# Performance work log

Measured on AMD Instinct MI355X. Metric: run time of the kernel, lower is better.

## Reference

```python
import jax, jax.numpy as jnp
import numpy as np

B, HH, WW, E = 8, 64, 64, 384
NH, EXP = 6, 2
D1 = (EXP * E) // NH * NH      # 768
HD = D1 // NH                  # 128
RPE = 512
LAYERS = 3
EPS = 1e-6


def srms(x):
    # SimpleRMSNorm: no learnable weight
    return x * jax.lax.rsqrt(jnp.mean(x * x, axis=-1, keepdims=True) + EPS)


def rpe_forward(pos, pw, pb, lw, lb, ow, ob):
    # pos: (n, 1) -> (n, NH*HD). Rpe MLP: act(pos_proj) -> layers x [norm,act,linear] -> out
    x = jax.nn.relu(pos @ pw + pb)
    for i in range(lw.shape[0]):  # fixed small layer count
        x = jax.nn.relu(srms(x)) @ lw[i] + lb[i]
    return jax.nn.relu(srms(x)) @ ow + ob


def tno_coeffs(n, pw, pb, lw, lb, ow, ob):
    # Toeplitz coeffs t_0..t_{n-1}, t_0(dummy), t_{-(n-1)}..t_{-1} for circular conv of len 2n
    pos = jnp.arange(1, n, dtype=jnp.float32)[:, None]             # (n-1, 1), par_type=1
    neg = -jnp.arange(1, n, dtype=jnp.float32)[::-1][:, None]      # -(n-1)..-1
    zero = jnp.zeros((1, 1), dtype=jnp.float32)
    t_zero = rpe_forward(zero, pw, pb, lw, lb, ow, ob)             # (1, NH*HD)
    t_pos = rpe_forward(pos, pw, pb, lw, lb, ow, ob)               # (n-1, NH*HD)
    t_neg = rpe_forward(neg, pw, pb, lw, lb, ow, ob)
    a = jnp.concatenate([t_zero, t_pos, t_zero, t_neg], axis=0)    # (2n, NH*HD)
    return a.reshape(2 * n, NH, HD).transpose(1, 0, 2)             # (NH, 2n, HD)


def tno_apply(v, a, axis):
    # v: (b, h, H, W, d); FFT-based Toeplitz (circular) mixing along `axis` in {-3, -2}
    n = v.shape[axis]
    a = a[:, :, None, :] if axis == -3 else a[:, None, :, :]
    y = jnp.fft.rfft(v, 2 * n, axis=axis)
    af = jnp.fft.rfft(a, 2 * n, axis=axis)
    out = jnp.fft.irfft(af * y, 2 * n, axis=axis)
    return jax.lax.slice_in_dim(out, 0, n, axis=out.ndim + axis)


def setup_inputs() -> dict:
    key = jax.random.key(0)
    ks = jax.random.split(key, 24)
    s = 0.02
    def rn(k, shape):
        return jax.random.normal(k, shape, dtype=jnp.float32) * s
    inp = {
        "x": jax.random.normal(ks[0], (B, HH, WW, E), dtype=jnp.float32),
        "H": HH, "W": WW,
        "Wu": rn(ks[1], (E, D1)), "bu": jnp.zeros((D1,), jnp.float32),
        "Wv": rn(ks[2], (E, D1)), "bv": jnp.zeros((D1,), jnp.float32),
        "Wo": rn(ks[3], (D1, E)), "bo": jnp.zeros((E,), jnp.float32),
    }
    for t, off in (("r1", 4), ("r2", 10)):
        inp[t + "_pw"] = rn(ks[off], (1, RPE))
        inp[t + "_pb"] = jnp.zeros((RPE,), jnp.float32)
        inp[t + "_lw"] = rn(ks[off + 1], (LAYERS, RPE, RPE))
        inp[t + "_lb"] = jnp.zeros((LAYERS, RPE), jnp.float32)
        inp[t + "_ow"] = rn(ks[off + 2], (RPE, NH * HD))
        inp[t + "_ob"] = jnp.zeros((NH * HD,), jnp.float32)
    return inp


def reference(x, H, W, Wu, bu, Wv, bv, Wo, bo,
              r1_pw, r1_pb, r1_lw, r1_lb, r1_ow, r1_ob,
              r2_pw, r2_pb, r2_lw, r2_lb, r2_ow, r2_ob):
    b = x.shape[0]
    xn = srms(x)                                    # pre_norm (SimpleRMSNorm)
    u = jax.nn.silu(xn @ Wu + bu)                   # gate branch
    v = jax.nn.silu(xn @ Wv + bv)
    v = v.reshape(b, H, W, NH, HD).transpose(0, 3, 1, 2, 4)        # b h H W d
    a_h = tno_coeffs(H, r2_pw, r2_pb, r2_lw, r2_lb, r2_ow, r2_ob)  # toep2, dim=-3
    a_w = tno_coeffs(W, r1_pw, r1_pb, r1_lw, r1_lb, r1_ow, r1_ob)  # toep1, dim=-2
    out = tno_apply(v, a_h, -3) + tno_apply(v, a_w, -2)
    out = out.transpose(0, 2, 3, 1, 4).reshape(b, H, W, NH * HD)   # b H W (h d)
    out = u * out
    return out @ Wo + bo + x
```

## Files before the change

### kernel.cpp

```cpp
#include <hip/hip_runtime.h>
#include <stdint.h>


typedef __attribute__((ext_vector_type(4))) float  f32x4;
typedef __attribute__((ext_vector_type(8))) short  s16x8;
typedef __attribute__((ext_vector_type(8))) unsigned short u16x8;
typedef __attribute__((ext_vector_type(4))) unsigned short u16x4;
typedef unsigned short u16;

#define M_TOT 32768

__device__ __forceinline__ u16 f2bf(float f) {
  union { float f; unsigned int u; } v; v.f = f;
  unsigned int r = (v.u + 0x7FFFu + ((v.u >> 16) & 1u)) >> 16;
  return (u16)r;
}
__device__ __forceinline__ float bf2f(u16 h) {
  union { unsigned int u; float f; } v; v.u = ((unsigned int)h) << 16;
  return v.f;
}
__device__ __forceinline__ float silu_f(float x) {
  return x * __builtin_amdgcn_rcpf(1.f + __expf(-x));
}

__device__ __forceinline__ void gload_lds16(const u16* g, u16* l) {
  __builtin_amdgcn_global_load_lds(
      (const __attribute__((address_space(1))) uint32_t*)g,
      (__attribute__((address_space(3))) uint32_t*)l, 16, 0, 0);
}

__global__ __launch_bounds__(256) void setup_k(
    const float* __restrict__ x, u16* __restrict__ xn,
    const float* __restrict__ Wu, const float* __restrict__ Wv,
    const float* __restrict__ Wo, u16* __restrict__ Wuvt, u16* __restrict__ Wot,
    const float* __restrict__ r1lw, const float* __restrict__ r1ow,
    const float* __restrict__ r2lw, const float* __restrict__ r2ow,
    u16* __restrict__ lwT, u16* __restrict__ owT,
    const float* __restrict__ r1pw, const float* __restrict__ r1pb,
    const float* __restrict__ r2pw, const float* __restrict__ r2pb,
    float* __restrict__ X0) {
  __shared__ float sm[32][33];
  const int bid = blockIdx.x;
  const int tid = threadIdx.x;

  if (bid < 8192) {
    int row  = bid * 4 + (tid >> 6);
    int lane = tid & 63;
    const float* xr = x + (size_t)row * 384 + lane;
    float v[6]; float ss = 0.f;
#pragma unroll
    for (int i = 0; i < 6; i++) { v[i] = xr[i * 64]; ss += v[i] * v[i]; }
#pragma unroll
    for (int off = 32; off > 0; off >>= 1) ss += __shfl_xor(ss, off);
    float sc = rsqrtf(ss * (1.f / 384.f) + 1e-6f);
    u16* o = xn + (size_t)row * 384 + lane;
#pragma unroll
    for (int i = 0; i < 6; i++) o[i * 64] = f2bf(v[i] * sc);
  } else if (bid < 11360) {
    int b = bid - 8192;
    const float* src; u16* dst; int C, DS, R0, C0;
    if (b < 2304) {
      int mlp = b / 1152, r = b % 1152;
      if (r < 768) {
        int L = r / 256, t = r % 256;
        R0 = (t / 16) * 32; C0 = (t % 16) * 32;
        src = (mlp ? r2lw : r1lw) + (size_t)L * 262144;
        dst = lwT + (size_t)(mlp * 3 + L) * 262144;
        C = 512; DS = 512;
      } else {
        int t = r - 768;
        R0 = (t / 24) * 32; C0 = (t % 24) * 32;
        src = mlp ? r2ow : r1ow;
        dst = owT + (size_t)mlp * 393216;
        C = 768; DS = 512;
      }
    } else {
      int t = b - 2304;
      if (t < 288)      { R0 = (t / 24) * 32; C0 = (t % 24) * 32;
                          src = Wu; C = 768; dst = Wuvt;             DS = 384; }
      else if (t < 576) { int t2 = t - 288; R0 = (t2 / 24) * 32; C0 = (t2 % 24) * 32;
                          src = Wv; C = 768; dst = Wuvt + 768 * 384; DS = 384; }
      else              { int t2 = t - 576; R0 = (t2 / 12) * 32; C0 = (t2 % 12) * 32;
                          src = Wo; C = 384; dst = Wot;              DS = 768; }
    }
    int lx = tid % 32, ly = tid / 32;
#pragma unroll
    for (int q = 0; q < 4; q++) {
      int y = q * 8 + ly;
      sm[y][lx] = src[(size_t)(R0 + y) * C + C0 + lx];
    }
    __syncthreads();
#pragma unroll
    for (int q = 0; q < 4; q++) {
      int y = q * 8 + ly;
      dst[(size_t)(C0 + y) * DS + R0 + lx] = f2bf(sm[lx][y]);
    }
  } else {
    int idx = (bid - 11360) * 256 + tid;
    int gid = idx * 4;
    int row = gid >> 9, col = gid & 511;
    int mlp = row >> 7, p = row & 127;
    float pos = (p < 64) ? (float)p : ((p == 64) ? 0.f : (float)(p - 128));
    const float* pw = (mlp ? r2pw : r1pw) + col;
    const float* pb = (mlp ? r2pb : r1pb) + col;
    f32x4 w = *(const f32x4*)pw;
    f32x4 bb = *(const f32x4*)pb;
    f32x4 o;
#pragma unroll
    for (int e = 0; e < 4; e++) o[e] = fmaxf(pos * w[e] + bb[e], 0.f);
    *(f32x4*)(X0 + gid) = o;
  }
}

template <int N, bool TOUT>
__global__ __launch_bounds__(256) void rpe_layer_k(
    const float* __restrict__ X,
    const u16* __restrict__ wtA, const u16* __restrict__ wtB,
    const float* __restrict__ bA, const float* __restrict__ bB,
    float* __restrict__ outA, float* __restrict__ outB) {
  constexpr int NT = N / 128;
  const int mlp = blockIdx.x / NT;
  const int n0  = (blockIdx.x % NT) * 128;
  const u16* WT = mlp ? wtB : wtA;
  const float* bias = mlp ? bB : bA;
  float* out = mlp ? outB : outA;
  const float* Xm = X + (size_t)mlp * 128 * 512;

  __shared__ float scale[128];
  __shared__ __align__(16) u16 As[128 * 64];
  __shared__ __align__(16) u16 Bs[128 * 64];

  const int tid  = threadIdx.x;
  const int lane = tid & 63;
  const int wid  = tid >> 6;
  const int wm   = wid >> 1, wn = wid & 1;
  const int fl   = lane & 15, fh = lane >> 4;

  {
    int row = tid >> 1, half = tid & 1;
    const float* xr = Xm + (size_t)row * 512 + half * 256;
    float ss = 0.f;
#pragma unroll 8
    for (int q = 0; q < 64; q++) {
      f32x4 v = *(const f32x4*)(xr + q * 4);
      ss += v[0] * v[0] + v[1] * v[1] + v[2] * v[2] + v[3] * v[3];
    }
    ss += __shfl_xor(ss, 1);
    if (!half) scale[row] = rsqrtf(ss * (1.f / 512.f) + 1e-6f);
  }
  __syncthreads();

  f32x4 acc[4][4];
  {
    f32x4 z = {0.f, 0.f, 0.f, 0.f};
#pragma unroll
    for (int i = 0; i < 4; i++)
#pragma unroll
      for (int j = 0; j < 4; j++) acc[i][j] = z;
  }

  const int arow = tid >> 1, acb = (tid & 1) * 32;
  const int sr = tid >> 3, sc = (tid & 7) * 8;

  for (int kt = 0; kt < 512; kt += 64) {
    {
      const float* xp = Xm + (size_t)arow * 512 + kt + acb;
      float s_ = scale[arow];
      u16* dst = As + arow * 64 + acb;
#pragma unroll
      for (int q = 0; q < 8; q++) {
        f32x4 v = *(const f32x4*)(xp + q * 4);
        u16x4 pk;
#pragma unroll
        for (int e = 0; e < 4; e++) pk[e] = f2bf(fmaxf(v[e], 0.f) * s_);
        *(u16x4*)(dst + q * 4) = pk;
      }
    }
    {
      const u16* gB = WT + (size_t)(n0 + sr) * 512 + kt + sc;
      u16* lB = Bs + sr * 64 + sc;
#pragma unroll
      for (int i = 0; i < 4; i++)
        gload_lds16(gB + (size_t)(i * 32) * 512, lB + i * 32 * 64);
    }
    __syncthreads();
#pragma unroll
    for (int ks = 0; ks < 2; ks++) {
      s16x8 af[4], bfr[4];
      const u16* ap = As + (wm * 64 + fl) * 64 + ks * 32 + fh * 8;
      const u16* bp = Bs + (wn * 64 + fl) * 64 + ks * 32 + fh * 8;
#pragma unroll
      for (int i = 0; i < 4; i++) af[i] = *(const s16x8*)(ap + i * 16 * 64);
#pragma unroll
      for (int j = 0; j < 4; j++) bfr[j] = *(const s16x8*)(bp + j * 16 * 64);
#pragma unroll
      for (int i = 0; i < 4; i++)
#pragma unroll
        for (int j = 0; j < 4; j++)
          acc[i][j] = __builtin_amdgcn_mfma_f32_16x16x32_bf16(af[i], bfr[j], acc[i][j], 0, 0, 0);
    }
    __syncthreads();
  }

#pragma unroll
  for (int i = 0; i < 4; i++)
#pragma unroll
    for (int j = 0; j < 4; j++) {
      int c = n0 + wn * 64 + j * 16 + fl;
      float bv_ = bias[c];
#pragma unroll
      for (int q = 0; q < 4; q++) {
        int r = wm * 64 + i * 16 + fh * 4 + q;
        if (TOUT) out[(size_t)c * 128 + r] = acc[i][j][q] + bv_;
        else      out[(size_t)r * N + c]   = acc[i][j][q] + bv_;
      }
    }
}

__global__ __launch_bounds__(256) void gemm0_k(
    const u16* __restrict__ A, const u16* __restrict__ Bt,
    u16* __restrict__ u_out, u16* __restrict__ vt_out,
    const float* __restrict__ bu, const float* __restrict__ bv) {
  __shared__ __align__(16) char smem[34816];
  u16*   As  = (u16*)smem;
  u16*   Bs  = As + 128 * 64;
  float* epi = (float*)smem;

  const int tid  = threadIdx.x;
  const int lane = tid & 63;
  const int wid  = tid >> 6;
  const int wm   = wid >> 1, wn = wid & 1;
  const int bm   = blockIdx.x & 255, bn = blockIdx.x >> 8;
  const int m0   = bm * 128, n0 = bn * 128;
  const int fl   = lane & 15, fh = lane >> 4;
  const int K    = 384;

  f32x4 acc[4][4];
  {
    f32x4 z = {0.f, 0.f, 0.f, 0.f};
#pragma unroll
    for (int i = 0; i < 4; i++)
#pragma unroll
      for (int j = 0; j < 4; j++) acc[i][j] = z;
  }

  const int sr  = tid >> 3;
  const int scl = (tid & 7) * 8;
  const int scs = ((tid & 7) ^ (sr & 7)) * 8;

  for (int kt = 0; kt < K; kt += 64) {
    const u16* gA = A  + (size_t)(m0 + sr) * K + kt + scs;
    const u16* gB = Bt + (size_t)(n0 + sr) * K + kt + scs;
    u16* lA = As + sr * 64 + scl;
    u16* lB = Bs + sr * 64 + scl;
#pragma unroll
    for (int i = 0; i < 4; i++) {
      gload_lds16(gA + (size_t)(i * 32) * K, lA + i * 32 * 64);
      gload_lds16(gB + (size_t)(i * 32) * K, lB + i * 32 * 64);
    }
    __syncthreads();
#pragma unroll
    for (int ks = 0; ks < 2; ks++) {
      s16x8 af[4], bfr[4];
      const int xc = ((ks * 4 + fh) ^ (fl & 7)) * 8;
      const u16* ap = As + (wm * 64 + fl) * 64 + xc;
      const u16* bp = Bs + (wn * 64 + fl) * 64 + xc;
#pragma unroll
      for (int i = 0; i < 4; i++) af[i] = *(const s16x8*)(ap + i * 16 * 64);
#pragma unroll
      for (int j = 0; j < 4; j++) bfr[j] = *(const s16x8*)(bp + j * 16 * 64);
#pragma unroll
      for (int i = 0; i < 4; i++)
#pragma unroll
        for (int j = 0; j < 4; j++)
          acc[i][j] = __builtin_amdgcn_mfma_f32_16x16x32_bf16(af[i], bfr[j], acc[i][j], 0, 0, 0);
    }
    __syncthreads();
  }

  for (int half = 0; half < 2; half++) {
    __syncthreads();
    if (wm == half) {
#pragma unroll
      for (int i = 0; i < 4; i++)
#pragma unroll
        for (int j = 0; j < 4; j++) {
          int er = i * 16 + fh * 4;
          int ec = wn * 64 + j * 16 + fl;
#pragma unroll
          for (int q = 0; q < 4; q++) epi[(er + q) * 132 + ec] = acc[i][j][q];
        }
    }
    __syncthreads();
    const bool isU = (n0 < 768);
    u16* baseo = isU ? u_out : vt_out;
    const int cc = tid >> 1;
    const int cg = (isU ? n0 : n0 - 768) + cc;
    const float bias_v = (isU ? bu : bv)[cg];
    u16* dst = baseo + (size_t)cg * M_TOT + m0 + half * 64;
#pragma unroll
    for (int q = 0; q < 4; q++) {
      int mb = (tid & 1) * 8 + q * 16;
      u16x8 pk;
#pragma unroll
      for (int e = 0; e < 8; e++) {
        int mm = mb + e;
        pk[e] = f2bf(silu_f(epi[mm * 132 + cc] + bias_v));
      }
      *(u16x8*)(dst + mb) = pk;
    }
  }
}

__global__ __launch_bounds__(512, 2) void gemm2_k(
    const u16* __restrict__ gT, const u16* __restrict__ Wot,
    float* __restrict__ out, const float* __restrict__ bo,
    const float* __restrict__ xres) {
  __shared__ __align__(16) u16 As[128 * 64];
  __shared__ __align__(16) u16 Bs[384 * 64];

  const int tid  = threadIdx.x;
  const int lane = tid & 63;
  const int wid  = tid >> 6;
  const int wm   = wid >> 2;
  const int wn   = wid & 3;
  const int m0   = blockIdx.x * 128;
  const int fl   = lane & 15, fh = lane >> 4;

  f32x4 acc[4][6];
  {
    f32x4 z = {0.f, 0.f, 0.f, 0.f};
#pragma unroll
    for (int i = 0; i < 4; i++)
#pragma unroll
      for (int j = 0; j < 6; j++) acc[i][j] = z;
  }

  const int sr  = tid >> 3;
  const int scl = (tid & 7) * 8;
  const int scs = ((tid & 7) ^ (sr & 7)) * 8;
  const int cr  = tid & 63;
  const int mw  = (tid >> 6) * 16;
  const int c8  = cr >> 3, of = cr & 7;

  for (int kt = 0; kt < 768; kt += 64) {
#pragma unroll
    for (int i = 0; i < 6; i++)
      gload_lds16(Wot + (size_t)(sr + 64 * i) * 768 + kt + scs,
                  Bs + (sr + 64 * i) * 64 + scl);
    {
      const u16* ga = gT + (size_t)(kt + cr) * M_TOT + m0 + mw;
      u16x8 r0 = *(const u16x8*)ga;
      u16x8 r1 = *(const u16x8*)(ga + 8);
#pragma unroll
      for (int e = 0; e < 8; e++)
        As[(mw + e) * 64 + ((c8 ^ e) << 3) + of] = r0[e];
#pragma unroll
      for (int e = 0; e < 8; e++)
        As[(mw + 8 + e) * 64 + ((c8 ^ e) << 3) + of] = r1[e];
    }
    __syncthreads();
#pragma unroll
    for (int ks = 0; ks < 2; ks++) {
      s16x8 af[4], bfr[6];
      const int xc = ((ks * 4 + fh) ^ (fl & 7)) * 8;
      const u16* ap = As + (wm * 64 + fl) * 64 + xc;
      const u16* bp = Bs + (wn * 96 + fl) * 64 + xc;
#pragma unroll
      for (int i = 0; i < 4; i++) af[i] = *(const s16x8*)(ap + i * 16 * 64);
#pragma unroll
      for (int j = 0; j < 6; j++) bfr[j] = *(const s16x8*)(bp + j * 16 * 64);
#pragma unroll
      for (int i = 0; i < 4; i++)
#pragma unroll
        for (int j = 0; j < 6; j++)
          acc[i][j] = __builtin_amdgcn_mfma_f32_16x16x32_bf16(af[i], bfr[j], acc[i][j], 0, 0, 0);
    }
    __syncthreads();
  }

  float bov[6];
#pragma unroll
  for (int j = 0; j < 6; j++) bov[j] = bo[wn * 96 + j * 16 + fl];
#pragma unroll
  for (int i = 0; i < 4; i++) {
#pragma unroll
    for (int q = 0; q < 4; q++) {
      int m = m0 + wm * 64 + i * 16 + fh * 4 + q;
      const float* xr = xres + (size_t)m * 384;
      float* orow = out + (size_t)m * 384;
#pragma unroll
      for (int j = 0; j < 6; j++) {
        int n = wn * 96 + j * 16 + fl;
        orow[n] = acc[i][j][q] + bov[j] + xr[n];
      }
    }
  }
}

__global__ __launch_bounds__(256) void conv_k(const u16* __restrict__ vt,
                                              const u16* __restrict__ ut,
                                              const float* __restrict__ a_hT,
                                              const float* __restrict__ a_wT,
                                              u16* __restrict__ gT) {
  __shared__ __align__(16) u16 Th[64 * 72];
  __shared__ __align__(16) u16 Tw[64 * 72];
  __shared__ __align__(16) u16 Vs[64 * 72];
  __shared__ __align__(16) u16 VTs[64 * 72];
  __shared__ __align__(16) u16 Us[64 * 72];
  __shared__ float ahr[192];
  __shared__ float awr[192];
  u16* epi = VTs;

  const int tid = threadIdx.x;
  const int c = blockIdx.x;
  const int lane = tid & 63, w = tid >> 6;
  const int fl = lane & 15, fh = lane >> 4;

  if (tid < 192) {
    int idx = (128 - tid) & 127;
    ahr[tid] = a_hT[(size_t)c * 128 + idx];
    awr[tid] = a_wT[(size_t)c * 128 + idx];
  }
  __syncthreads();

  {
    int y = tid & 63, j0 = (tid >> 6) * 16;
    int base = 128 - y + j0;
    u16x8 p0, p1, q0, q1;
#pragma unroll
    for (int e = 0; e < 8; e++) {
      p0[e] = f2bf(ahr[base + e]);
      p1[e] = f2bf(ahr[base + 8 + e]);
      q0[e] = f2bf(awr[base + e]);
      q1[e] = f2bf(awr[base + 8 + e]);
    }
    *(u16x8*)(Th + y * 72 + j0)     = p0;
    *(u16x8*)(Th + y * 72 + j0 + 8) = p1;
    *(u16x8*)(Tw + y * 72 + j0)     = q0;
    *(u16x8*)(Tw + y * 72 + j0 + 8) = q1;
  }

  const int sy = tid >> 2, sx = (tid & 3) * 16;
  const int ty = tid & 63, tj = (tid >> 6) * 16;

  for (int b = 0; b < 8; b++) {
    const u16* srcv = vt + (size_t)c * M_TOT + b * 4096;
    const u16* srcu = ut + (size_t)c * M_TOT + b * 4096;
    *(u16x8*)(Vs + sy * 72 + sx)     = *(const u16x8*)(srcv + sy * 64 + sx);
    *(u16x8*)(Vs + sy * 72 + sx + 8) = *(const u16x8*)(srcv + sy * 64 + sx + 8);
    *(u16x8*)(Us + sy * 72 + sx)     = *(const u16x8*)(srcu + sy * 64 + sx);
    *(u16x8*)(Us + sy * 72 + sx + 8) = *(const u16x8*)(srcu + sy * 64 + sx + 8);
    __syncthreads();

    {
      u16x8 q0 = *(const u16x8*)(Vs + ty * 72 + tj);
      u16x8 q1 = *(const u16x8*)(Vs + ty * 72 + tj + 8);
#pragma unroll
      for (int e = 0; e < 8; e++) VTs[(tj + e) * 72 + ty]     = q0[e];
#pragma unroll
      for (int e = 0; e < 8; e++) VTs[(tj + 8 + e) * 72 + ty] = q1[e];
    }
    __syncthreads();

    f32x4 acc[4];
    {
      f32x4 z = {0.f, 0.f, 0.f, 0.f};
#pragma unroll
      for (int i = 0; i < 4; i++) acc[i] = z;
    }
#pragma unroll
    for (int ks = 0; ks < 2; ks++) {
      s16x8 qh = *(const s16x8*)(Th + (w * 16 + fl) * 72 + ks * 32 + fh * 8);
#pragma unroll
      for (int i = 0; i < 4; i++) {
        s16x8 p = *(const s16x8*)(VTs + (i * 16 + fl) * 72 + ks * 32 + fh * 8);
        acc[i] = __builtin_amdgcn_mfma_f32_16x16x32_bf16(p, qh, acc[i], 0, 0, 0);
      }
      s16x8 qw = *(const s16x8*)(Vs + (w * 16 + fl) * 72 + ks * 32 + fh * 8);
#pragma unroll
      for (int i = 0; i < 4; i++) {
        s16x8 p = *(const s16x8*)(Tw + (i * 16 + fl) * 72 + ks * 32 + fh * 8);
        acc[i] = __builtin_amdgcn_mfma_f32_16x16x32_bf16(p, qw, acc[i], 0, 0, 0);
      }
    }
    __syncthreads();

    {
      int y = w * 16 + fl;
#pragma unroll
      for (int i = 0; i < 4; i++) {
        u16x4 uq = *(const u16x4*)(Us + y * 72 + i * 16 + fh * 4);
        u16x4 pk;
#pragma unroll
        for (int e = 0; e < 4; e++) pk[e] = f2bf(acc[i][e] * bf2f(uq[e]));
        *(u16x4*)(epi + y * 72 + i * 16 + fh * 4) = pk;
      }
    }
    __syncthreads();

    {
      u16x8 a0 = *(const u16x8*)(epi + sy * 72 + sx);
      u16x8 a1 = *(const u16x8*)(epi + sy * 72 + sx + 8);
      u16* dst = gT + (size_t)c * M_TOT + b * 4096 + sy * 64 + sx;
      *(u16x8*)dst = a0;
      *(u16x8*)(dst + 8) = a1;
    }
    __syncthreads();
  }
}

extern "C" void kernel_launch(void* const* d_in, const int* in_sizes, int n_in,
                              void* d_out, int out_size, void* d_ws, size_t ws_size,
                              hipStream_t stream) {
  const float* x    = (const float*)d_in[0];
  const float* Wu   = (const float*)d_in[3];
  const float* bu   = (const float*)d_in[4];
  const float* Wv   = (const float*)d_in[5];
  const float* bv   = (const float*)d_in[6];
  const float* Wo   = (const float*)d_in[7];
  const float* bo   = (const float*)d_in[8];
  const float* r1pw = (const float*)d_in[9];
  const float* r1pb = (const float*)d_in[10];
  const float* r1lw = (const float*)d_in[11];
  const float* r1lb = (const float*)d_in[12];
  const float* r1ow = (const float*)d_in[13];
  const float* r1ob = (const float*)d_in[14];
  const float* r2pw = (const float*)d_in[15];
  const float* r2pb = (const float*)d_in[16];
  const float* r2lw = (const float*)d_in[17];
  const float* r2lb = (const float*)d_in[18];
  const float* r2ow = (const float*)d_in[19];
  const float* r2ob = (const float*)d_in[20];
  float* outp = (float*)d_out;

  char* ws = (char*)d_ws;
  size_t off = 0;
  auto carve = [&](size_t bytes) {
    char* p = ws + off;
    off += (bytes + 255) & ~(size_t)255;
    return p;
  };
  u16*   xn   = (u16*)carve((size_t)M_TOT * 384 * 2);
  u16*   uT   = (u16*)carve((size_t)768 * M_TOT * 2);
  u16*   vT   = (u16*)carve((size_t)768 * M_TOT * 2);
  u16*   gT   = (u16*)carve((size_t)768 * M_TOT * 2);
  u16*   Wuvt = (u16*)carve((size_t)1536 * 384 * 2);
  u16*   Wot  = (u16*)carve((size_t)384 * 768 * 2);
  float* awT  = (float*)carve((size_t)768 * 128 * 4);
  float* ahT  = (float*)carve((size_t)768 * 128 * 4);

  char* rb  = (char*)gT;
  u16*   lwT = (u16*)rb;
  u16*   owT = (u16*)(rb + 3145728);
  float* X0  = (float*)(rb + 3145728 + 1572864);
  float* X1  = X0 + 256 * 512;

  setup_k<<<11488, 256, 0, stream>>>(x, xn, Wu, Wv, Wo, Wuvt, Wot,
                                     r1lw, r1ow, r2lw, r2ow, lwT, owT,
                                     r1pw, r1pb, r2pw, r2pb, X0);

  rpe_layer_k<512, false><<<8, 256, 0, stream>>>(X0, lwT, lwT + 3 * 262144,
                                                 r1lb, r2lb, X1, X1 + 128 * 512);
  rpe_layer_k<512, false><<<8, 256, 0, stream>>>(X1, lwT + 262144, lwT + 4 * 262144,
                                                 r1lb + 512, r2lb + 512, X0, X0 + 128 * 512);
  rpe_layer_k<512, false><<<8, 256, 0, stream>>>(X0, lwT + 2 * 262144, lwT + 5 * 262144,
                                                 r1lb + 1024, r2lb + 1024, X1, X1 + 128 * 512);
  rpe_layer_k<768, true><<<12, 256, 0, stream>>>(X1, owT, owT + 393216,
                                                 r1ob, r2ob, awT, ahT);

  gemm0_k<<<256 * 12, 256, 0, stream>>>(xn, Wuvt, uT, vT, bu, bv);
  conv_k<<<768, 256, 0, stream>>>(vT, uT, ahT, awT, gT);
  gemm2_k<<<256, 512, 0, stream>>>(gT, Wot, outp, bo, x);
}
```

Before: 395.9 us.

## Restructure RPE layer kernel with full weight slice in LDS and double-buffered A

The RPE MLP layer kernel now uses 64-column output slices, which doubles the grid from 8/12 to 16/24 blocks. Each block preloads its whole 64x512 weight slice into LDS with an XOR swizzle, and double-buffers the normalized activation tiles with register prefetch, so only one barrier is needed per k-step. The gemm2 A-tile transpose load is also reworked to issue one 16-byte load per thread per pass, with each lane reading a different M chunk. The aim is better parallelism in tiny, latency-bound kernels and fewer LDS bank conflicts, at the cost of more LDS per block.

```diff
diff --git a/kernel.cpp b/kernel.cpp
--- a/kernel.cpp
+++ b/kernel.cpp
@@ -118,23 +118,30 @@
     const u16* __restrict__ wtA, const u16* __restrict__ wtB,
     const float* __restrict__ bA, const float* __restrict__ bB,
     float* __restrict__ outA, float* __restrict__ outB) {
-  constexpr int NT = N / 128;
-  const int mlp = blockIdx.x / NT;
-  const int n0  = (blockIdx.x % NT) * 128;
+  constexpr int NSL = N / 64;
+  const int mlp = blockIdx.x / NSL;
+  const int n0  = (blockIdx.x % NSL) * 64;
   const u16* WT = mlp ? wtB : wtA;
   const float* bias = mlp ? bB : bA;
   float* out = mlp ? outB : outA;
   const float* Xm = X + (size_t)mlp * 128 * 512;
 
+  __shared__ __align__(16) u16 Bs[64 * 512];
+  __shared__ __align__(16) u16 As[2][128 * 64];
   __shared__ float scale[128];
-  __shared__ __align__(16) u16 As[128 * 64];
-  __shared__ __align__(16) u16 Bs[128 * 64];
 
   const int tid  = threadIdx.x;
   const int lane = tid & 63;
-  const int wid  = tid >> 6;
-  const int wm   = wid >> 1, wn = wid & 1;
+  const int w    = tid >> 6;
   const int fl   = lane & 15, fh = lane >> 4;
+
+#pragma unroll
+  for (int r = 0; r < 16; r++) {
+    int row  = r * 4 + w;
+    int csrc = (lane & ~7) | ((lane & 7) ^ (row & 7));
+    gload_lds16(WT + (size_t)(n0 + row) * 512 + csrc * 8,
+                Bs + row * 512 + lane * 8);
+  }
 
   {
     int row = tid >> 1, half = tid & 1;
@@ -150,67 +157,89 @@
   }
   __syncthreads();
 
-  f32x4 acc[4][4];
+  int arow[4], akc[4];
+  float s_[4];
+#pragma unroll
+  for (int q = 0; q < 4; q++) {
+    int cid = q * 256 + tid;
+    arow[q] = cid >> 3;
+    akc[q]  = cid & 7;
+    s_[q]   = scale[arow[q]];
+  }
+
+#pragma unroll
+  for (int q = 0; q < 4; q++) {
+    const float* xp = Xm + (size_t)arow[q] * 512 + akc[q] * 8;
+    f32x4 v0 = *(const f32x4*)xp;
+    f32x4 v1 = *(const f32x4*)(xp + 4);
+    u16x8 pk;
+#pragma unroll
+    for (int e = 0; e < 4; e++) pk[e]     = f2bf(fmaxf(v0[e], 0.f) * s_[q]);
+#pragma unroll
+    for (int e = 0; e < 4; e++) pk[4 + e] = f2bf(fmaxf(v1[e], 0.f) * s_[q]);
+    *(u16x8*)(&As[0][arow[q] * 64 + ((akc[q] ^ (arow[q] & 7)) * 8)]) = pk;
+  }
+  __syncthreads();
+
+  f32x4 acc[2][4];
   {
     f32x4 z = {0.f, 0.f, 0.f, 0.f};
 #pragma unroll
-    for (int i = 0; i < 4; i++)
+    for (int i = 0; i < 2; i++)
 #pragma unroll
       for (int j = 0; j < 4; j++) acc[i][j] = z;
   }
 
-  const int arow = tid >> 1, acb = (tid & 1) * 32;
-  const int sr = tid >> 3, sc = (tid & 7) * 8;
-
-  for (int kt = 0; kt < 512; kt += 64) {
-    {
-      const float* xp = Xm + (size_t)arow * 512 + kt + acb;
-      float s_ = scale[arow];
-      u16* dst = As + arow * 64 + acb;
-#pragma unroll
-      for (int q = 0; q < 8; q++) {
-        f32x4 v = *(const f32x4*)(xp + q * 4);
-        u16x4 pk;
-#pragma unroll
-        for (int e = 0; e < 4; e++) pk[e] = f2bf(fmaxf(v[e], 0.f) * s_);
-        *(u16x4*)(dst + q * 4) = pk;
-      }
-    }
-    {
-      const u16* gB = WT + (size_t)(n0 + sr) * 512 + kt + sc;
-      u16* lB = Bs + sr * 64 + sc;
-#pragma unroll
-      for (int i = 0; i < 4; i++)
-        gload_lds16(gB + (size_t)(i * 32) * 512, lB + i * 32 * 64);
-    }
-    __syncthreads();
+  for (int kti = 0; kti < 8; kti++) {
+    const int cur = kti & 1;
+    f32x4 pf0[4], pf1[4];
+    if (kti < 7) {
+#pragma unroll
+      for (int q = 0; q < 4; q++) {
+        const float* xp = Xm + (size_t)arow[q] * 512 + (kti + 1) * 64 + akc[q] * 8;
+        pf0[q] = *(const f32x4*)xp;
+        pf1[q] = *(const f32x4*)(xp + 4);
+      }
+    }
 #pragma unroll
     for (int ks = 0; ks < 2; ks++) {
-      s16x8 af[4], bfr[4];
-      const u16* ap = As + (wm * 64 + fl) * 64 + ks * 32 + fh * 8;
-      const u16* bp = Bs + (wn * 64 + fl) * 64 + ks * 32 + fh * 8;
-#pragma unroll
-      for (int i = 0; i < 4; i++) af[i] = *(const s16x8*)(ap + i * 16 * 64);
-#pragma unroll
-      for (int j = 0; j < 4; j++) bfr[j] = *(const s16x8*)(bp + j * 16 * 64);
-#pragma unroll
-      for (int i = 0; i < 4; i++)
+      const int xc = ((ks * 4 + fh) ^ (fl & 7)) * 8;
+      s16x8 af[2], bfr[4];
+#pragma unroll
+      for (int i = 0; i < 2; i++)
+        af[i] = *(const s16x8*)(&As[cur][(w * 32 + i * 16 + fl) * 64 + xc]);
+#pragma unroll
+      for (int j = 0; j < 4; j++)
+        bfr[j] = *(const s16x8*)(&Bs[(j * 16 + fl) * 512 + kti * 64 + xc]);
+#pragma unroll
+      for (int i = 0; i < 2; i++)
 #pragma unroll
         for (int j = 0; j < 4; j++)
           acc[i][j] = __builtin_amdgcn_mfma_f32_16x16x32_bf16(af[i], bfr[j], acc[i][j], 0, 0, 0);
     }
-    __syncthreads();
-  }
-
-#pragma unroll
-  for (int i = 0; i < 4; i++)
+    if (kti < 7) {
+#pragma unroll
+      for (int q = 0; q < 4; q++) {
+        u16x8 pk;
+#pragma unroll
+        for (int e = 0; e < 4; e++) pk[e]     = f2bf(fmaxf(pf0[q][e], 0.f) * s_[q]);
+#pragma unroll
+        for (int e = 0; e < 4; e++) pk[4 + e] = f2bf(fmaxf(pf1[q][e], 0.f) * s_[q]);
+        *(u16x8*)(&As[cur ^ 1][arow[q] * 64 + ((akc[q] ^ (arow[q] & 7)) * 8)]) = pk;
+      }
+    }
+    __syncthreads();
+  }
+
+#pragma unroll
+  for (int i = 0; i < 2; i++)
 #pragma unroll
     for (int j = 0; j < 4; j++) {
-      int c = n0 + wn * 64 + j * 16 + fl;
+      int c = n0 + j * 16 + fl;
       float bv_ = bias[c];
 #pragma unroll
       for (int q = 0; q < 4; q++) {
-        int r = wm * 64 + i * 16 + fh * 4 + q;
+        int r = w * 32 + i * 16 + fh * 4 + q;
         if (TOUT) out[(size_t)c * 128 + r] = acc[i][j][q] + bv_;
         else      out[(size_t)r * N + c]   = acc[i][j][q] + bv_;
       }
@@ -339,25 +368,23 @@
   const int sr  = tid >> 3;
   const int scl = (tid & 7) * 8;
   const int scs = ((tid & 7) ^ (sr & 7)) * 8;
-  const int cr  = tid & 63;
-  const int mw  = (tid >> 6) * 16;
-  const int c8  = cr >> 3, of = cr & 7;
 
   for (int kt = 0; kt < 768; kt += 64) {
 #pragma unroll
     for (int i = 0; i < 6; i++)
       gload_lds16(Wot + (size_t)(sr + 64 * i) * 768 + kt + scs,
                   Bs + (sr + 64 * i) * 64 + scl);
-    {
-      const u16* ga = gT + (size_t)(kt + cr) * M_TOT + m0 + mw;
-      u16x8 r0 = *(const u16x8*)ga;
-      u16x8 r1 = *(const u16x8*)(ga + 8);
+#pragma unroll
+    for (int r = 0; r < 2; r++) {
+      int cid = r * 512 + tid;
+      int row = cid >> 4;
+      int cm  = cid & 15;
+      const u16* ga = gT + (size_t)(kt + row) * M_TOT + m0 + cm * 8;
+      u16x8 rv = *(const u16x8*)ga;
+      int kc = row >> 3, of = row & 7;
 #pragma unroll
       for (int e = 0; e < 8; e++)
-        As[(mw + e) * 64 + ((c8 ^ e) << 3) + of] = r0[e];
-#pragma unroll
-      for (int e = 0; e < 8; e++)
-        As[(mw + 8 + e) * 64 + ((c8 ^ e) << 3) + of] = r1[e];
+        As[(cm * 8 + e) * 64 + ((kc ^ e) << 3) + of] = rv[e];
     }
     __syncthreads();
 #pragma unroll
@@ -560,13 +587,13 @@
                                      r1lw, r1ow, r2lw, r2ow, lwT, owT,
                                      r1pw, r1pb, r2pw, r2pb, X0);
 
-  rpe_layer_k<512, false><<<8, 256, 0, stream>>>(X0, lwT, lwT + 3 * 262144,
-                                                 r1lb, r2lb, X1, X1 + 128 * 512);
-  rpe_layer_k<512, false><<<8, 256, 0, stream>>>(X1, lwT + 262144, lwT + 4 * 262144,
-                                                 r1lb + 512, r2lb + 512, X0, X0 + 128 * 512);
-  rpe_layer_k<512, false><<<8, 256, 0, stream>>>(X0, lwT + 2 * 262144, lwT + 5 * 262144,
-                                                 r1lb + 1024, r2lb + 1024, X1, X1 + 128 * 512);
-  rpe_layer_k<768, true><<<12, 256, 0, stream>>>(X1, owT, owT + 393216,
+  rpe_layer_k<512, false><<<16, 256, 0, stream>>>(X0, lwT, lwT + 3 * 262144,
+                                                  r1lb, r2lb, X1, X1 + 128 * 512);
+  rpe_layer_k<512, false><<<16, 256, 0, stream>>>(X1, lwT + 262144, lwT + 4 * 262144,
+                                                  r1lb + 512, r2lb + 512, X0, X0 + 128 * 512);
+  rpe_layer_k<512, false><<<16, 256, 0, stream>>>(X0, lwT + 2 * 262144, lwT + 5 * 262144,
+                                                  r1lb + 1024, r2lb + 1024, X1, X1 + 128 * 512);
+  rpe_layer_k<768, true><<<24, 256, 0, stream>>>(X1, owT, owT + 393216,
                                                  r1ob, r2ob, awT, ahT);
 
   gemm0_k<<<256 * 12, 256, 0, stream>>>(xn, Wuvt, uT, vT, bu, bv);
```

Result: faster. 366.3 us (-7.5%).
